# Optimization experiments

Measured on AMD Instinct MI355X. Metric: run time of the kernel, lower is better.

## Reference

```python
import jax, jax.numpy as jnp
import numpy as np

N, E, D_IN, D_H, D_OUT = 50000, 800000, 128, 128, 64


def _glorot(key, shape):
    fan_in, fan_out = shape[1], shape[0]
    lim = (6.0 / (fan_in + fan_out)) ** 0.5
    return jax.random.uniform(key, shape, jnp.float32, -lim, lim)


def setup_inputs() -> dict:
    key = jax.random.key(0)
    ks = jax.random.split(key, 8)
    x = jax.random.normal(ks[0], (N, D_IN), jnp.float32)
    edge_index = jax.random.randint(ks[1], (2, E), 0, N, jnp.int64)
    # SAGEConv layer 1: lin_l (on aggregated neighbors, with bias) and lin_r (root, no bias)
    W1l = _glorot(ks[2], (D_H, D_IN))
    b1 = jnp.zeros((D_H,), jnp.float32)
    W1r = _glorot(ks[3], (D_H, D_IN))
    # SAGEConv layer 2
    W2l = _glorot(ks[4], (D_OUT, D_H))
    b2 = jnp.zeros((D_OUT,), jnp.float32)
    W2r = _glorot(ks[5], (D_OUT, D_H))
    return {"x": x, "edge_index": edge_index, "W1l": W1l, "b1": b1, "W1r": W1r,
            "W2l": W2l, "b2": b2, "W2r": W2r}


def _sage_conv(x, src, dst, inv_deg, Wl, b, Wr):
    # mean-aggregate neighbor features: gather x[src], scatter-sum into dst, divide by degree
    msg_sum = jax.ops.segment_sum(x[src], dst, num_segments=N)  # [N, d]
    agg = msg_sum * inv_deg[:, None]
    return agg @ Wl.T + b + x @ Wr.T


def reference(x, edge_index, W1l, b1, W1r, W2l, b2, W2r):
    src, dst = edge_index[0], edge_index[1]
    deg = jax.ops.segment_sum(jnp.ones((E,), jnp.float32), dst, num_segments=N)
    inv_deg = jnp.where(deg > 0, 1.0 / jnp.maximum(deg, 1.0), 0.0)
    h = _sage_conv(x, src, dst, inv_deg, W1l, b1, W1r)
    h = jax.nn.relu(h)  # dropout is identity in eval mode
    out = _sage_conv(h, src, dst, inv_deg, W2l, b2, W2r)
    return out
```

## Files before the change

kernel.cpp:

```cpp
#include <hip/hip_runtime.h>
#include <hip/hip_bf16.h>

typedef __hip_bfloat16 bf16;
typedef __attribute__((ext_vector_type(8))) short short8;
typedef __attribute__((ext_vector_type(4))) float f32x4;
typedef unsigned short u16;

#define N_NODES 50000
#define NE      800000
#define DIN     128
#define DH      128
#define DOUT    64
#define MTILES  (N_NODES / 16)
#define CAP     64
#define DSTRIDE 32
#define NXCD    8
#define NPX     (N_NODES / NXCD)
#define ECHUNK  2048
#define NCHUNK  ((NE + ECHUNK - 1) / ECHUNK)
#define SCAT_BLKS (NCHUNK * NXCD)

__device__ __forceinline__ int clamp_node(int s) {
    return min(max(s, 0), N_NODES - 1);
}
__device__ __forceinline__ float b2f(short s) {
    unsigned u = ((unsigned)(unsigned short)s) << 16;
    float f; __builtin_memcpy(&f, &u, 4); return f;
}
__device__ __forceinline__ short f2b(float f) {
    __hip_bfloat16 h = __float2bfloat16(f);
    short s; __builtin_memcpy(&s, &h, 2); return s;
}

__global__ void k_build(const int* __restrict__ src, const int* __restrict__ dst,
                        int* __restrict__ degPad, u16* __restrict__ csrPad,
                        const float* __restrict__ x, __hip_bfloat162* __restrict__ xb2,
                        const float* __restrict__ W1l, const float* __restrict__ W1r,
                        const float* __restrict__ W2l, const float* __restrict__ W2r,
                        bf16* __restrict__ W1b, bf16* __restrict__ W2b) {
    int b = blockIdx.x;
    if (b < SCAT_BLKS) {
        int chunk = b >> 3;
        int lo = (b & 7) * NPX, hi = lo + NPX;
        int e0 = chunk * ECHUNK + threadIdx.x * 8;
        if (e0 + 7 < NE) {
            int4 d0 = *(const int4*)(dst + e0);
            int4 d1 = *(const int4*)(dst + e0 + 4);
            int4 s0 = *(const int4*)(src + e0);
            int4 s1 = *(const int4*)(src + e0 + 4);
            int dv[8] = {d0.x, d0.y, d0.z, d0.w, d1.x, d1.y, d1.z, d1.w};
            int sv[8] = {s0.x, s0.y, s0.z, s0.w, s1.x, s1.y, s1.z, s1.w};
            #pragma unroll
            for (int j = 0; j < 8; ++j) {
                int t = dv[j];
                if (t >= lo && t < hi) {
                    int pos = atomicAdd(&degPad[t * DSTRIDE], 1);
                    if (pos < CAP) csrPad[t * CAP + pos] = (u16)sv[j];
                }
            }
        }
    } else if (b < SCAT_BLKS + 6250) {
        int i = (b - SCAT_BLKS) * 256 + threadIdx.x;
        float4 v = ((const float4*)x)[i];
        __hip_bfloat162 a, bb;
        a.x = __float2bfloat16(v.x); a.y = __float2bfloat16(v.y);
        bb.x = __float2bfloat16(v.z); bb.y = __float2bfloat16(v.w);
        xb2[2 * i]     = a;
        xb2[2 * i + 1] = bb;
    } else {
        int i = (b - SCAT_BLKS - 6250) * 256 + threadIdx.x;
        if (i < 128 * 256) {
            int n = i >> 8, k = i & 255;
            float v = (k < 128) ? W1l[n * 128 + k] : W1r[n * 128 + (k - 128)];
            W1b[i] = __float2bfloat16(v);
        } else {
            int j = i - 128 * 256;
            int n = j >> 7, k = j & 127;
            float v = (n < 64) ? W2l[n * 128 + k] : W2r[(n - 64) * 128 + k];
            W2b[j] = __float2bfloat16(v);
        }
    }
}

__global__ __launch_bounds__(256) void k_agg1(const int* __restrict__ degPad, const u16* __restrict__ csrPad,
                                              const short* __restrict__ xb,
                                              short* __restrict__ msg) {
    int node = blockIdx.x * 4 + (threadIdx.x >> 6);
    if (node >= N_NODES) return;
    int lane = threadIdx.x & 63;
    int g = lane >> 4, c = lane & 15;
    int d = min(max(degPad[node * DSTRIDE], 0), CAP);
    int lo = node * CAP, hi = lo + d;
    float acc[8];
    #pragma unroll
    for (int j = 0; j < 8; ++j) acc[j] = 0.f;
    int i = lo;
    for (; i + 15 < hi; i += 16) {
        int n0 = clamp_node(csrPad[i + g]);
        int n1 = clamp_node(csrPad[i + 4 + g]);
        int n2 = clamp_node(csrPad[i + 8 + g]);
        int n3 = clamp_node(csrPad[i + 12 + g]);
        short8 v0 = *(const short8*)(xb + (size_t)n0 * DIN + c * 8);
        short8 v1 = *(const short8*)(xb + (size_t)n1 * DIN + c * 8);
        short8 v2 = *(const short8*)(xb + (size_t)n2 * DIN + c * 8);
        short8 v3 = *(const short8*)(xb + (size_t)n3 * DIN + c * 8);
        #pragma unroll
        for (int j = 0; j < 8; ++j)
            acc[j] += (b2f(v0[j]) + b2f(v1[j])) + (b2f(v2[j]) + b2f(v3[j]));
    }
    for (; i + 7 < hi; i += 8) {
        int n0 = clamp_node(csrPad[i + g]);
        int n1 = clamp_node(csrPad[i + 4 + g]);
        short8 v0 = *(const short8*)(xb + (size_t)n0 * DIN + c * 8);
        short8 v1 = *(const short8*)(xb + (size_t)n1 * DIN + c * 8);
        #pragma unroll
        for (int j = 0; j < 8; ++j) acc[j] += b2f(v0[j]) + b2f(v1[j]);
    }
    for (; i < hi; i += 4) {
        bool valid = (i + g) < hi;
        int n = clamp_node(csrPad[valid ? (i + g) : i]);
        short8 v = *(const short8*)(xb + (size_t)n * DIN + c * 8);
        if (valid) {
            #pragma unroll
            for (int j = 0; j < 8; ++j) acc[j] += b2f(v[j]);
        }
    }
    #pragma unroll
    for (int j = 0; j < 8; ++j) {
        acc[j] += __shfl_xor(acc[j], 16);
        acc[j] += __shfl_xor(acc[j], 32);
    }
    if (g == 0) {
        float inv = (d > 0) ? 1.0f / (float)d : 0.0f;
        short8 o;
        #pragma unroll
        for (int j = 0; j < 8; ++j) o[j] = f2b(acc[j] * inv);
        *(short8*)(msg + (size_t)node * DIN + c * 8) = o;
    }
}

__global__ __launch_bounds__(256) void k_mfma12(const short* __restrict__ msg,
                                                const short* __restrict__ xb,
                                                const short* __restrict__ W1b,
                                                const float* __restrict__ b1,
                                                const short* __restrict__ W2b,
                                                bf16* __restrict__ pb,
                                                float* __restrict__ qbuf) {
    __shared__ short hs[16][136];
    int wave = threadIdx.x >> 6, lane = threadIdx.x & 63;
    int q = lane >> 4, mr = lane & 15;
    int n0 = wave * 32;
    short8 Bf1[2][8];
    #pragma unroll
    for (int t = 0; t < 2; ++t) {
        const short* wrow = W1b + (size_t)(n0 + t * 16 + mr) * 256 + q * 8;
        #pragma unroll
        for (int ks = 0; ks < 8; ++ks) Bf1[t][ks] = *(const short8*)(wrow + ks * 32);
    }
    short8 Bf2[2][4];
    #pragma unroll
    for (int t = 0; t < 2; ++t) {
        const short* wrow = W2b + (size_t)(n0 + t * 16 + mr) * 128 + q * 8;
        #pragma unroll
        for (int ks = 0; ks < 4; ++ks) Bf2[t][ks] = *(const short8*)(wrow + ks * 32);
    }
    float bias0 = b1[n0 + mr], bias1 = b1[n0 + 16 + mr];
    for (int mt = blockIdx.x; mt < MTILES; mt += gridDim.x) {
        const short* a0 = msg + (size_t)(mt * 16 + mr) * DIN + q * 8;
        const short* a1 = xb  + (size_t)(mt * 16 + mr) * DIN + q * 8;
        short8 Af[8];
        #pragma unroll
        for (int ks = 0; ks < 4; ++ks) Af[ks]     = *(const short8*)(a0 + ks * 32);
        #pragma unroll
        for (int ks = 0; ks < 4; ++ks) Af[4 + ks] = *(const short8*)(a1 + ks * 32);
        f32x4 acc0 = {0.f, 0.f, 0.f, 0.f}, acc1 = {0.f, 0.f, 0.f, 0.f};
        #pragma unroll
        for (int ks = 0; ks < 8; ++ks) {
            acc0 = __builtin_amdgcn_mfma_f32_16x16x32_bf16(Af[ks], Bf1[0][ks], acc0, 0, 0, 0);
            acc1 = __builtin_amdgcn_mfma_f32_16x16x32_bf16(Af[ks], Bf1[1][ks], acc1, 0, 0, 0);
        }
        __syncthreads();
        #pragma unroll
        for (int r = 0; r < 4; ++r) {
            int row = q * 4 + r;
            float v0 = acc0[r] + bias0;
            float v1 = acc1[r] + bias1;
            hs[row][n0 + mr]      = f2b(v0 > 0.f ? v0 : 0.f);
            hs[row][n0 + 16 + mr] = f2b(v1 > 0.f ? v1 : 0.f);
        }
        __syncthreads();
        short8 Ah[4];
        #pragma unroll
        for (int ks = 0; ks < 4; ++ks) Ah[ks] = *(const short8*)(&hs[mr][ks * 32 + q * 8]);
        f32x4 c20 = {0.f, 0.f, 0.f, 0.f}, c21 = {0.f, 0.f, 0.f, 0.f};
        #pragma unroll
        for (int ks = 0; ks < 4; ++ks) {
            c20 = __builtin_amdgcn_mfma_f32_16x16x32_bf16(Ah[ks], Bf2[0][ks], c20, 0, 0, 0);
            c21 = __builtin_amdgcn_mfma_f32_16x16x32_bf16(Ah[ks], Bf2[1][ks], c21, 0, 0, 0);
        }
        #pragma unroll
        for (int r = 0; r < 4; ++r) {
            int row = mt * 16 + q * 4 + r;
            int c0 = n0 + mr, c1 = n0 + 16 + mr;
            if (c0 < 64) {
                pb[(size_t)row * 64 + c0] = __float2bfloat16(c20[r]);
                pb[(size_t)row * 64 + c1] = __float2bfloat16(c21[r]);
            } else {
                qbuf[(size_t)row * 64 + (c0 - 64)] = c20[r];
                qbuf[(size_t)row * 64 + (c1 - 64)] = c21[r];
            }
        }
    }
}

__global__ __launch_bounds__(256) void k_agg2f(const int* __restrict__ degPad, const u16* __restrict__ csrPad,
                                               const short* __restrict__ pb, const float* __restrict__ qbuf,
                                               const float* __restrict__ b2, float* __restrict__ out) {
    int node = blockIdx.x * 4 + (threadIdx.x >> 6);
    if (node >= N_NODES) return;
    int lane = threadIdx.x & 63;
    int g = lane >> 3, c = lane & 7;
    int d = min(max(degPad[node * DSTRIDE], 0), CAP);
    int lo = node * CAP, hi = lo + d;
    float acc[8];
    #pragma unroll
    for (int j = 0; j < 8; ++j) acc[j] = 0.f;
    int i = lo;
    for (; i + 31 < hi; i += 32) {
        int n0 = clamp_node(csrPad[i + g]);
        int n1 = clamp_node(csrPad[i + 8 + g]);
        int n2 = clamp_node(csrPad[i + 16 + g]);
        int n3 = clamp_node(csrPad[i + 24 + g]);
        short8 v0 = *(const short8*)(pb + (size_t)n0 * 64 + c * 8);
        short8 v1 = *(const short8*)(pb + (size_t)n1 * 64 + c * 8);
        short8 v2 = *(const short8*)(pb + (size_t)n2 * 64 + c * 8);
        short8 v3 = *(const short8*)(pb + (size_t)n3 * 64 + c * 8);
        #pragma unroll
        for (int j = 0; j < 8; ++j)
            acc[j] += (b2f(v0[j]) + b2f(v1[j])) + (b2f(v2[j]) + b2f(v3[j]));
    }
    for (; i + 15 < hi; i += 16) {
        int n0 = clamp_node(csrPad[i + g]);
        int n1 = clamp_node(csrPad[i + 8 + g]);
        short8 v0 = *(const short8*)(pb + (size_t)n0 * 64 + c * 8);
        short8 v1 = *(const short8*)(pb + (size_t)n1 * 64 + c * 8);
        #pragma unroll
        for (int j = 0; j < 8; ++j) acc[j] += b2f(v0[j]) + b2f(v1[j]);
    }
    for (; i < hi; i += 8) {
        bool valid = (i + g) < hi;
        int n = clamp_node(csrPad[valid ? (i + g) : i]);
        short8 v = *(const short8*)(pb + (size_t)n * 64 + c * 8);
        if (valid) {
            #pragma unroll
            for (int j = 0; j < 8; ++j) acc[j] += b2f(v[j]);
        }
    }
    #pragma unroll
    for (int j = 0; j < 8; ++j) {
        acc[j] += __shfl_xor(acc[j], 8);
        acc[j] += __shfl_xor(acc[j], 16);
        acc[j] += __shfl_xor(acc[j], 32);
    }
    if (g == 0) {
        float inv = (d > 0) ? 1.0f / (float)d : 0.0f;
        const float* qr = qbuf + (size_t)node * 64 + c * 8;
        const float* br = b2 + c * 8;
        float* orow = out + (size_t)node * 64 + c * 8;
        float4 o0, o1;
        o0.x = acc[0] * inv + qr[0] + br[0];
        o0.y = acc[1] * inv + qr[1] + br[1];
        o0.z = acc[2] * inv + qr[2] + br[2];
        o0.w = acc[3] * inv + qr[3] + br[3];
        o1.x = acc[4] * inv + qr[4] + br[4];
        o1.y = acc[5] * inv + qr[5] + br[5];
        o1.z = acc[6] * inv + qr[6] + br[6];
        o1.w = acc[7] * inv + qr[7] + br[7];
        ((float4*)orow)[0] = o0;
        ((float4*)orow)[1] = o1;
    }
}

extern "C" void kernel_launch(void* const* d_in, const int* in_sizes, int n_in,
                              void* d_out, int out_size, void* d_ws, size_t ws_size,
                              hipStream_t stream) {
    const float* x   = (const float*)d_in[0];
    const int*   ei  = (const int*)  d_in[1];
    const float* W1l = (const float*)d_in[2];
    const float* b1  = (const float*)d_in[3];
    const float* W1r = (const float*)d_in[4];
    const float* W2l = (const float*)d_in[5];
    const float* b2  = (const float*)d_in[6];
    const float* W2r = (const float*)d_in[7];
    float* out = (float*)d_out;

    const int* src = ei;
    const int* dst = ei + NE;

    char* ws = (char*)d_ws;
    int*   degPad = (int*)  (ws + 0);
    u16*   csrPad = (u16*)  (ws + 6400000);
    short* xb     = (short*)(ws + 12800000);
    short* msg    = (short*)(ws + 25600000);
    bf16*  pb     = (bf16*) (ws + 38400000);
    float* qbuf   = (float*)(ws + 44800000);
    bf16*  W1b    = (bf16*) (ws + 57600000);
    bf16*  W2b    = (bf16*) (ws + 57665536);

    hipMemsetAsync(degPad, 0, 6400000, stream);

    k_build<<<SCAT_BLKS + 6250 + 192, 256, 0, stream>>>(src, dst, degPad, csrPad,
                                                        x, (__hip_bfloat162*)xb,
                                                        W1l, W1r, W2l, W2r, W1b, W2b);
    k_agg1<<<(N_NODES + 3) / 4, 256, 0, stream>>>(degPad, csrPad, xb, msg);
    k_mfma12<<<512, 256, 0, stream>>>(msg, xb, (const short*)W1b, b1, (const short*)W2b, pb, qbuf);
    k_agg2f<<<(N_NODES + 3) / 4, 256, 0, stream>>>(degPad, csrPad, (const short*)pb, qbuf, b2, out);
}
```

Before: 194.5 us.

## Bucket CSR neighbor lists by source range to improve gather locality

```diff
diff --git a/kernel.cpp b/kernel.cpp
--- a/kernel.cpp
+++ b/kernel.cpp
@@ -12,7 +12,10 @@
 #define DH      128
 #define DOUT    64
 #define MTILES  (N_NODES / 16)
-#define CAP     64
+#define NBKT    4
+#define BRNG    12500
+#define BCAP    24
+#define SLOTS   (NBKT * BCAP)
 #define DSTRIDE 32
 #define NXCD    8
 #define NPX     (N_NODES / NXCD)
@@ -54,8 +57,10 @@
             for (int j = 0; j < 8; ++j) {
                 int t = dv[j];
                 if (t >= lo && t < hi) {
-                    int pos = atomicAdd(&degPad[t * DSTRIDE], 1);
-                    if (pos < CAP) csrPad[t * CAP + pos] = (u16)sv[j];
+                    int sc = clamp_node(sv[j]);
+                    int bkt = sc / BRNG;
+                    int pos = atomicAdd(&degPad[t * DSTRIDE + bkt], 1);
+                    if (pos < BCAP) csrPad[t * SLOTS + bkt * BCAP + pos] = (u16)sv[j];
                 }
             }
         }
@@ -89,40 +94,34 @@
     if (node >= N_NODES) return;
     int lane = threadIdx.x & 63;
     int g = lane >> 4, c = lane & 15;
-    int d = min(max(degPad[node * DSTRIDE], 0), CAP);
-    int lo = node * CAP, hi = lo + d;
+    int4 db4 = *(const int4*)(degPad + node * DSTRIDE);
+    int degs[4] = {db4.x, db4.y, db4.z, db4.w};
     float acc[8];
     #pragma unroll
     for (int j = 0; j < 8; ++j) acc[j] = 0.f;
-    int i = lo;
-    for (; i + 15 < hi; i += 16) {
-        int n0 = clamp_node(csrPad[i + g]);
-        int n1 = clamp_node(csrPad[i + 4 + g]);
-        int n2 = clamp_node(csrPad[i + 8 + g]);
-        int n3 = clamp_node(csrPad[i + 12 + g]);
-        short8 v0 = *(const short8*)(xb + (size_t)n0 * DIN + c * 8);
-        short8 v1 = *(const short8*)(xb + (size_t)n1 * DIN + c * 8);
-        short8 v2 = *(const short8*)(xb + (size_t)n2 * DIN + c * 8);
-        short8 v3 = *(const short8*)(xb + (size_t)n3 * DIN + c * 8);
-        #pragma unroll
-        for (int j = 0; j < 8; ++j)
-            acc[j] += (b2f(v0[j]) + b2f(v1[j])) + (b2f(v2[j]) + b2f(v3[j]));
-    }
-    for (; i + 7 < hi; i += 8) {
-        int n0 = clamp_node(csrPad[i + g]);
-        int n1 = clamp_node(csrPad[i + 4 + g]);
-        short8 v0 = *(const short8*)(xb + (size_t)n0 * DIN + c * 8);
-        short8 v1 = *(const short8*)(xb + (size_t)n1 * DIN + c * 8);
-        #pragma unroll
-        for (int j = 0; j < 8; ++j) acc[j] += b2f(v0[j]) + b2f(v1[j]);
-    }
-    for (; i < hi; i += 4) {
-        bool valid = (i + g) < hi;
-        int n = clamp_node(csrPad[valid ? (i + g) : i]);
-        short8 v = *(const short8*)(xb + (size_t)n * DIN + c * 8);
-        if (valid) {
+    int dsum = 0;
+    #pragma unroll
+    for (int b = 0; b < NBKT; ++b) {
+        int d_b = min(max(degs[b], 0), BCAP);
+        dsum += d_b;
+        int lo = node * SLOTS + b * BCAP, hi = lo + d_b;
+        int i = lo;
+        for (; i + 7 < hi; i += 8) {
+            int n0 = clamp_node(csrPad[i + g]);
+            int n1 = clamp_node(csrPad[i + 4 + g]);
+            short8 v0 = *(const short8*)(xb + (size_t)n0 * DIN + c * 8);
+            short8 v1 = *(const short8*)(xb + (size_t)n1 * DIN + c * 8);
             #pragma unroll
-            for (int j = 0; j < 8; ++j) acc[j] += b2f(v[j]);
+            for (int j = 0; j < 8; ++j) acc[j] += b2f(v0[j]) + b2f(v1[j]);
+        }
+        for (; i < hi; i += 4) {
+            bool valid = (i + g) < hi;
+            int n = clamp_node(csrPad[valid ? (i + g) : i]);
+            short8 v = *(const short8*)(xb + (size_t)n * DIN + c * 8);
+            if (valid) {
+                #pragma unroll
+                for (int j = 0; j < 8; ++j) acc[j] += b2f(v[j]);
+            }
         }
     }
     #pragma unroll
@@ -131,7 +130,7 @@
         acc[j] += __shfl_xor(acc[j], 32);
     }
     if (g == 0) {
-        float inv = (d > 0) ? 1.0f / (float)d : 0.0f;
+        float inv = (dsum > 0) ? 1.0f / (float)dsum : 0.0f;
         short8 o;
         #pragma unroll
         for (int j = 0; j < 8; ++j) o[j] = f2b(acc[j] * inv);
@@ -220,40 +219,34 @@
     if (node >= N_NODES) return;
     int lane = threadIdx.x & 63;
     int g = lane >> 3, c = lane & 7;
-    int d = min(max(degPad[node * DSTRIDE], 0), CAP);
-    int lo = node * CAP, hi = lo + d;
+    int4 db4 = *(const int4*)(degPad + node * DSTRIDE);
+    int degs[4] = {db4.x, db4.y, db4.z, db4.w};
     float acc[8];
     #pragma unroll
     for (int j = 0; j < 8; ++j) acc[j] = 0.f;
-    int i = lo;
-    for (; i + 31 < hi; i += 32) {
-        int n0 = clamp_node(csrPad[i + g]);
-        int n1 = clamp_node(csrPad[i + 8 + g]);
-        int n2 = clamp_node(csrPad[i + 16 + g]);
-        int n3 = clamp_node(csrPad[i + 24 + g]);
-        short8 v0 = *(const short8*)(pb + (size_t)n0 * 64 + c * 8);
-        short8 v1 = *(const short8*)(pb + (size_t)n1 * 64 + c * 8);
-        short8 v2 = *(const short8*)(pb + (size_t)n2 * 64 + c * 8);
-        short8 v3 = *(const short8*)(pb + (size_t)n3 * 64 + c * 8);
-        #pragma unroll
-        for (int j = 0; j < 8; ++j)
-            acc[j] += (b2f(v0[j]) + b2f(v1[j])) + (b2f(v2[j]) + b2f(v3[j]));
-    }
-    for (; i + 15 < hi; i += 16) {
-        int n0 = clamp_node(csrPad[i + g]);
-        int n1 = clamp_node(csrPad[i + 8 + g]);
-        short8 v0 = *(const short8*)(pb + (size_t)n0 * 64 + c * 8);
-        short8 v1 = *(const short8*)(pb + (size_t)n1 * 64 + c * 8);
-        #pragma unroll
-        for (int j = 0; j < 8; ++j) acc[j] += b2f(v0[j]) + b2f(v1[j]);
-    }
-    for (; i < hi; i += 8) {
-        bool valid = (i + g) < hi;
-        int n = clamp_node(csrPad[valid ? (i + g) : i]);
-        short8 v = *(const short8*)(pb + (size_t)n * 64 + c * 8);
-        if (valid) {
+    int dsum = 0;
+    #pragma unroll
+    for (int b = 0; b < NBKT; ++b) {
+        int d_b = min(max(degs[b], 0), BCAP);
+        dsum += d_b;
+        int lo = node * SLOTS + b * BCAP, hi = lo + d_b;
+        int i = lo;
+        for (; i + 15 < hi; i += 16) {
+            int n0 = clamp_node(csrPad[i + g]);
+            int n1 = clamp_node(csrPad[i + 8 + g]);
+            short8 v0 = *(const short8*)(pb + (size_t)n0 * 64 + c * 8);
+            short8 v1 = *(const short8*)(pb + (size_t)n1 * 64 + c * 8);
             #pragma unroll
-            for (int j = 0; j < 8; ++j) acc[j] += b2f(v[j]);
+            for (int j = 0; j < 8; ++j) acc[j] += b2f(v0[j]) + b2f(v1[j]);
+        }
+        for (; i < hi; i += 8) {
+            bool valid = (i + g) < hi;
+            int n = clamp_node(csrPad[valid ? (i + g) : i]);
+            short8 v = *(const short8*)(pb + (size_t)n * 64 + c * 8);
+            if (valid) {
+                #pragma unroll
+                for (int j = 0; j < 8; ++j) acc[j] += b2f(v[j]);
+            }
         }
     }
     #pragma unroll
@@ -263,7 +256,7 @@
         acc[j] += __shfl_xor(acc[j], 32);
     }
     if (g == 0) {
-        float inv = (d > 0) ? 1.0f / (float)d : 0.0f;
+        float inv = (dsum > 0) ? 1.0f / (float)dsum : 0.0f;
         const float* qr = qbuf + (size_t)node * 64 + c * 8;
         const float* br = b2 + c * 8;
         float* orow = out + (size_t)node * 64 + c * 8;
@@ -300,12 +293,12 @@
     char* ws = (char*)d_ws;
     int*   degPad = (int*)  (ws + 0);
     u16*   csrPad = (u16*)  (ws + 6400000);
-    short* xb     = (short*)(ws + 12800000);
-    short* msg    = (short*)(ws + 25600000);
-    bf16*  pb     = (bf16*) (ws + 38400000);
-    float* qbuf   = (float*)(ws + 44800000);
-    bf16*  W1b    = (bf16*) (ws + 57600000);
-    bf16*  W2b    = (bf16*) (ws + 57665536);
+    short* xb     = (short*)(ws + 16000000);
+    short* msg    = (short*)(ws + 28800000);
+    bf16*  pb     = (bf16*) (ws + 41600000);
+    float* qbuf   = (float*)(ws + 48000000);
+    bf16*  W1b    = (bf16*) (ws + 60800000);
+    bf16*  W2b    = (bf16*) (ws + 60865536);
 
     hipMemsetAsync(degPad, 0, 6400000, stream);
 
@@ -313,6 +306,6 @@
                                                         x, (__hip_bfloat162*)xb,
                                                         W1l, W1r, W2l, W2r, W1b, W2b);
     k_agg1<<<(N_NODES + 3) / 4, 256, 0, stream>>>(degPad, csrPad, xb, msg);
-    k_mfma12<<<512, 256, 0, stream>>>(msg, xb, (const short*)W1b, b1, (const short*)W2b, pb, qbuf);
+    k_mfma12<<<1024, 256, 0, stream>>>(msg, xb, (const short*)W1b, b1, (const short*)W2b, pb, qbuf);
     k_agg2f<<<(N_NODES + 3) / 4, 256, 0, stream>>>(degPad, csrPad, (const short*)pb, qbuf, b2, out);
 }
```

Measured after the change: 226.2 us. 16.3% more time.
